# Optimization experiments

Hardware: AMD Instinct MI355X
Metric: run time of the kernel (lower is better)

## Reference

```python
import jax, jax.numpy as jnp
import numpy as np

PENALTY_FACTOR = 2.0
THRESHOLD = 0.01
PHASE_INT_THRESHOLD = 0.01  # hard-coded 0.01 in the original forward


def setup_inputs() -> dict:
    key = jax.random.key(0)
    k1, k2, k3 = jax.random.split(key, 3)
    B, twoN = 1024, 65536
    prediction = jax.random.normal(k1, (B, twoN), dtype=jnp.float32)
    label = jax.random.normal(k2, (B, twoN), dtype=jnp.float32)
    spectrogram = jax.random.normal(k3, (B, 128, 128), dtype=jnp.float32)
    return {"prediction": prediction, "label": label, "spectrogram": spectrogram}


def _significant_bounds(mask, n):
    # mask: [B, N] bool. first/last index where mask is True; (0, n-1) if none.
    idx = jnp.arange(n)
    any_ = jnp.any(mask, axis=1, keepdims=True)
    first = jnp.min(jnp.where(mask, idx, n), axis=1, keepdims=True)
    last = jnp.max(jnp.where(mask, idx, -1), axis=1, keepdims=True)
    first = jnp.where(any_, first, 0)
    last = jnp.where(any_, last, n - 1)
    return first, last  # each [B, 1]


def reference(prediction, label, spectrogram):
    B, two_n = label.shape
    n = two_n // 2
    label_real, label_imag = label[:, :n], label[:, n:]
    pred_real, pred_imag = prediction[:, :n], prediction[:, n:]

    label_phase = jnp.arctan2(label_imag, label_real)
    pred_phase = jnp.arctan2(pred_imag, pred_real)
    label_int = label_real ** 2 + label_imag ** 2
    pred_int = pred_real ** 2 + pred_imag ** 2

    idx = jnp.arange(n)[None, :]  # [1, N]
    fr, lr = _significant_bounds(jnp.abs(label_real) > THRESHOLD, n)
    fi, li = _significant_bounds(jnp.abs(label_imag) > THRESHOLD, n)

    # penalty applied outside the significant region [first, last]
    scale_r = jnp.where((idx < fr) | (idx > lr), PENALTY_FACTOR, 1.0)
    scale_i = jnp.where((idx < fi) | (idx > li), PENALTY_FACTOR, 1.0)

    mse_real = (pred_real - label_real) ** 2 * scale_r
    mse_imag = (pred_imag - label_imag) ** 2 * scale_i
    mse_int = (pred_int - label_int) ** 2
    mse_phase = jnp.where(jnp.abs(label_int) < PHASE_INT_THRESHOLD,
                          0.0, (pred_phase - label_phase) ** 2)

    per_sample = (mse_real.mean(axis=1) + mse_imag.mean(axis=1)
                  + 10.0 * mse_int.mean(axis=1) + 5.0 * mse_phase.mean(axis=1))
    return per_sample.mean()
```

## Files before the change

kernel.cpp:

```cpp
#include <hip/hip_runtime.h>
#include <math.h>

#define SIG_THRESHOLD 0.01f
#define PHASE_INT_THR 0.01f

__device__ __forceinline__ float fast_atan2f(float y, float x) {
    float ax = fabsf(x), ay = fabsf(y);
    float mx = fmaxf(ax, ay), mn = fminf(ax, ay);
    float t = mn * __builtin_amdgcn_rcpf(mx);
    t = (mx == 0.0f) ? 0.0f : t;
    float s = t * t;
    float p =        -0.01172120f;
    p = fmaf(s, p,    0.05265332f);
    p = fmaf(s, p,   -0.11643287f);
    p = fmaf(s, p,    0.19354346f);
    p = fmaf(s, p,   -0.33262347f);
    p = fmaf(s, p,    0.99997726f);
    float r = p * t;
    r = (ay > ax) ? (1.57079632679f - r) : r;
    r = (x < 0.0f) ? (3.14159265359f - r) : r;
    return copysignf(r, y);
}


__device__ __forceinline__ float waveReduceSum(float v) {
#pragma unroll
    for (int o = 32; o > 0; o >>= 1) v += __shfl_down(v, o, 64);
    return v;
}
__device__ __forceinline__ int waveReduceMin(int v) {
#pragma unroll
    for (int o = 32; o > 0; o >>= 1) v = min(v, __shfl_down(v, o, 64));
    return v;
}
__device__ __forceinline__ int waveReduceMax(int v) {
#pragma unroll
    for (int o = 32; o > 0; o >>= 1) v = max(v, __shfl_down(v, o, 64));
    return v;
}

__device__ __forceinline__ float blockReduceSum(float v, float* lds) {
    __syncthreads();
    v = waveReduceSum(v);
    int lane = threadIdx.x & 63, wave = threadIdx.x >> 6;
    if (lane == 0) lds[wave] = v;
    __syncthreads();
    int nw = (blockDim.x + 63) >> 6;
    float r = (threadIdx.x < nw) ? lds[threadIdx.x] : 0.0f;
    if (threadIdx.x < 64) r = waveReduceSum(r);
    if (threadIdx.x == 0) lds[0] = r;
    __syncthreads();
    return lds[0];
}
__device__ __forceinline__ int blockReduceMin(int v, int* lds) {
    __syncthreads();
    v = waveReduceMin(v);
    int lane = threadIdx.x & 63, wave = threadIdx.x >> 6;
    if (lane == 0) lds[wave] = v;
    __syncthreads();
    int nw = (blockDim.x + 63) >> 6;
    int r = (threadIdx.x < nw) ? lds[threadIdx.x] : 0x7fffffff;
    if (threadIdx.x < 64) r = waveReduceMin(r);
    if (threadIdx.x == 0) lds[0] = r;
    __syncthreads();
    return lds[0];
}
__device__ __forceinline__ int blockReduceMax(int v, int* lds) {
    __syncthreads();
    v = waveReduceMax(v);
    int lane = threadIdx.x & 63, wave = threadIdx.x >> 6;
    if (lane == 0) lds[wave] = v;
    __syncthreads();
    int nw = (blockDim.x + 63) >> 6;
    int r = (threadIdx.x < nw) ? lds[threadIdx.x] : (int)0x80000000;
    if (threadIdx.x < 64) r = waveReduceMax(r);
    if (threadIdx.x == 0) lds[0] = r;
    __syncthreads();
    return lds[0];
}

#define COARSE_SENT (1 << 29)

__device__ __forceinline__ void process4(float4 lrv, float4 liv, float4 prv, float4 piv,
                                         int v,
                                         float& sum_r, float& sum_i, float& sum_int, float& sum_ph,
                                         int& cfr4, int& clr4, int& cfi4, int& cli4) {
#pragma unroll
    for (int k = 0; k < 4; ++k) {
        float lrk = (&lrv.x)[k], lik = (&liv.x)[k];
        float prk = (&prv.x)[k], pik = (&piv.x)[k];

        float dr = prk - lrk;  sum_r += dr * dr;
        float di = pik - lik;  sum_i += di * di;

        float lint = fmaf(lrk, lrk, lik * lik);
        float pint = fmaf(prk, prk, pik * pik);
        float dint = pint - lint;  sum_int += dint * dint;

        float dph = fast_atan2f(pik, prk) - fast_atan2f(lik, lrk);
        sum_ph += (lint >= PHASE_INT_THR) ? dph * dph : 0.0f;
    }
    float amr = fmaxf(fmaxf(fabsf(lrv.x), fabsf(lrv.y)), fmaxf(fabsf(lrv.z), fabsf(lrv.w)));
    float ami = fmaxf(fmaxf(fabsf(liv.x), fabsf(liv.y)), fmaxf(fabsf(liv.z), fabsf(liv.w)));
    bool sr = amr > SIG_THRESHOLD;
    bool si = ami > SIG_THRESHOLD;
    cfr4 = min(cfr4, sr ? v : COARSE_SENT);
    clr4 = sr ? v : clr4;
    cfi4 = min(cfi4, si ? v : COARSE_SENT);
    cli4 = si ? v : cli4;
}

__global__ void __launch_bounds__(512)
prl_row_kernel(const float* __restrict__ pred, const float* __restrict__ label,
               float* __restrict__ row_out, int n, int two_n) {
    __shared__ float s_f[16];
    __shared__ int s_i[16];
    __shared__ int s_b[4];

    const int row = blockIdx.x;
    const float* __restrict__ P = pred  + (size_t)row * two_n;
    const float* __restrict__ L = label + (size_t)row * two_n;

    const int tid = threadIdx.x;
    const int nt  = blockDim.x;

    const float4* __restrict__ Lr4 = reinterpret_cast<const float4*>(L);
    const float4* __restrict__ Li4 = reinterpret_cast<const float4*>(L + n);
    const float4* __restrict__ Pr4 = reinterpret_cast<const float4*>(P);
    const float4* __restrict__ Pi4 = reinterpret_cast<const float4*>(P + n);

    float sum_r = 0.f, sum_i = 0.f, sum_int = 0.f, sum_ph = 0.f;
    int cfr4 = COARSE_SENT, clr4 = -1, cfi4 = COARSE_SENT, cli4 = -1;

    const int nvec  = n / 4;
    const int iters = nvec / (2 * nt);
    int v = tid;
    for (int it = 0; it < iters; ++it, v += 2 * nt) {
        const int v1 = v + nt;
        float4 a0 = Lr4[v],  b0 = Li4[v],  c0 = Pr4[v],  d0 = Pi4[v];
        float4 a1 = Lr4[v1], b1 = Li4[v1], c1 = Pr4[v1], d1 = Pi4[v1];
        process4(a0, b0, c0, d0, v,  sum_r, sum_i, sum_int, sum_ph, cfr4, clr4, cfi4, cli4);
        process4(a1, b1, c1, d1, v1, sum_r, sum_i, sum_int, sum_ph, cfr4, clr4, cfi4, cli4);
    }

    float tot_r   = blockReduceSum(sum_r, s_f);
    float tot_i   = blockReduceSum(sum_i, s_f);
    float tot_int = blockReduceSum(sum_int, s_f);
    float tot_ph  = blockReduceSum(sum_ph, s_f);

    int fr4 = blockReduceMin(cfr4, s_i);
    int lr4 = blockReduceMax(clr4, s_i);
    int fi4 = blockReduceMin(cfi4, s_i);
    int li4 = blockReduceMax(cli4, s_i);

    if (tid < 4) s_b[tid] = (tid & 1) ? -1 : n;
    __syncthreads();
    if (tid < 16) {
        int which = tid >> 2;
        int k = tid & 3;
        const float* base = (which >= 2) ? (L + n) : L;
        int v4 = (which == 0) ? fr4 : (which == 1) ? lr4 : (which == 2) ? fi4 : li4;
        bool valid = (which & 1) ? (v4 >= 0) : (v4 < COARSE_SENT);
        if (valid) {
            int idx = v4 * 4 + k;
            if (fabsf(base[idx]) > SIG_THRESHOLD) {
                if (which & 1) atomicMax(&s_b[which], idx);
                else           atomicMin(&s_b[which], idx);
            }
        }
    }
    __syncthreads();
    int fr = s_b[0], lr = s_b[1], fi = s_b[2], li = s_b[3];
    if (fr == n) { fr = 0; lr = n - 1; }
    if (fi == n) { fi = 0; li = n - 1; }

    float o_r = 0.f, o_i = 0.f;
    for (int i = tid; i < fr; i += nt)          { float d = P[i] - L[i];         o_r += d * d; }
    for (int i = lr + 1 + tid; i < n; i += nt)  { float d = P[i] - L[i];         o_r += d * d; }
    for (int i = tid; i < fi; i += nt)          { float d = P[n + i] - L[n + i]; o_i += d * d; }
    for (int i = li + 1 + tid; i < n; i += nt)  { float d = P[n + i] - L[n + i]; o_i += d * d; }

    float tot_or = blockReduceSum(o_r, s_f);
    float tot_oi = blockReduceSum(o_i, s_f);

    if (tid == 0) {
        float wr = tot_r + tot_or;
        float wi = tot_i + tot_oi;
        float per_sample = (wr + wi + 10.0f * tot_int + 5.0f * tot_ph) / (float)n;
        row_out[row] = per_sample;
    }
}

__global__ void __launch_bounds__(1024)
prl_finalize_kernel(const float* __restrict__ rows, float* __restrict__ out, int B) {
    __shared__ float s_f[16];
    float v = 0.f;
    for (int i = threadIdx.x; i < B; i += blockDim.x) v += rows[i];
    float t = blockReduceSum(v, s_f);
    if (threadIdx.x == 0) out[0] = t / (float)B;
}

extern "C" void kernel_launch(void* const* d_in, const int* in_sizes, int n_in,
                              void* d_out, int out_size, void* d_ws, size_t ws_size,
                              hipStream_t stream) {
    const float* pred  = (const float*)d_in[0];
    const float* label = (const float*)d_in[1];

    const int B     = in_sizes[2] / (128 * 128);
    const int two_n = in_sizes[0] / B;
    const int n     = two_n / 2;

    float* row_out = (float*)d_ws;
    float* out     = (float*)d_out;

    prl_row_kernel<<<B, 512, 0, stream>>>(pred, label, row_out, n, two_n);
    prl_finalize_kernel<<<1, 1024, 0, stream>>>(row_out, out, B);
}
```

Baseline: 114.1 us.

## Software-pipeline row loads and compute phase difference with a single atan2

```diff
diff --git a/kernel.cpp b/kernel.cpp
--- a/kernel.cpp
+++ b/kernel.cpp
@@ -3,6 +3,7 @@
 
 #define SIG_THRESHOLD 0.01f
 #define PHASE_INT_THR 0.01f
+#define TWO_PI_F 6.283185307179586f
 
 __device__ __forceinline__ float fast_atan2f(float y, float x) {
     float ax = fabsf(x), ay = fabsf(y);
@@ -90,14 +91,21 @@
         float lrk = (&lrv.x)[k], lik = (&liv.x)[k];
         float prk = (&prv.x)[k], pik = (&piv.x)[k];
 
-        float dr = prk - lrk;  sum_r += dr * dr;
-        float di = pik - lik;  sum_i += di * di;
+        float dr = prk - lrk;  sum_r = fmaf(dr, dr, sum_r);
+        float di = pik - lik;  sum_i = fmaf(di, di, sum_i);
 
         float lint = fmaf(lrk, lrk, lik * lik);
         float pint = fmaf(prk, prk, pik * pik);
-        float dint = pint - lint;  sum_int += dint * dint;
-
-        float dph = fast_atan2f(pik, prk) - fast_atan2f(lik, lrk);
+        float dint = pint - lint;  sum_int = fmaf(dint, dint, sum_int);
+
+        float cross = fmaf(pik, lrk, -(prk * lik));
+        float dotv  = fmaf(prk, lrk,   pik * lik);
+        float w = fast_atan2f(cross, dotv);
+        bool php = pik > 0.0f;
+        bool phl = lik > 0.0f;
+        float sigma = (php && !phl && w < 0.0f) ?  1.0f
+                    : ((!php && phl && w > 0.0f) ? -1.0f : 0.0f);
+        float dph = fmaf(sigma, TWO_PI_F, w);
         sum_ph += (lint >= PHASE_INT_THR) ? dph * dph : 0.0f;
     }
     float amr = fmaxf(fmaxf(fabsf(lrv.x), fabsf(lrv.y)), fmaxf(fabsf(lrv.z), fabsf(lrv.w)));
@@ -110,38 +118,14 @@
     cli4 = si ? v : cli4;
 }
 
-__global__ void __launch_bounds__(512)
-prl_row_kernel(const float* __restrict__ pred, const float* __restrict__ label,
-               float* __restrict__ row_out, int n, int two_n) {
-    __shared__ float s_f[16];
-    __shared__ int s_i[16];
-    __shared__ int s_b[4];
-
-    const int row = blockIdx.x;
-    const float* __restrict__ P = pred  + (size_t)row * two_n;
-    const float* __restrict__ L = label + (size_t)row * two_n;
-
+__device__ __forceinline__ void row_epilogue(const float* __restrict__ P,
+                                             const float* __restrict__ L,
+                                             float* __restrict__ row_out, int row, int n,
+                                             float sum_r, float sum_i, float sum_int, float sum_ph,
+                                             int cfr4, int clr4, int cfi4, int cli4,
+                                             float* s_f, int* s_i, int* s_b) {
     const int tid = threadIdx.x;
     const int nt  = blockDim.x;
-
-    const float4* __restrict__ Lr4 = reinterpret_cast<const float4*>(L);
-    const float4* __restrict__ Li4 = reinterpret_cast<const float4*>(L + n);
-    const float4* __restrict__ Pr4 = reinterpret_cast<const float4*>(P);
-    const float4* __restrict__ Pi4 = reinterpret_cast<const float4*>(P + n);
-
-    float sum_r = 0.f, sum_i = 0.f, sum_int = 0.f, sum_ph = 0.f;
-    int cfr4 = COARSE_SENT, clr4 = -1, cfi4 = COARSE_SENT, cli4 = -1;
-
-    const int nvec  = n / 4;
-    const int iters = nvec / (2 * nt);
-    int v = tid;
-    for (int it = 0; it < iters; ++it, v += 2 * nt) {
-        const int v1 = v + nt;
-        float4 a0 = Lr4[v],  b0 = Li4[v],  c0 = Pr4[v],  d0 = Pi4[v];
-        float4 a1 = Lr4[v1], b1 = Li4[v1], c1 = Pr4[v1], d1 = Pi4[v1];
-        process4(a0, b0, c0, d0, v,  sum_r, sum_i, sum_int, sum_ph, cfr4, clr4, cfi4, cli4);
-        process4(a1, b1, c1, d1, v1, sum_r, sum_i, sum_int, sum_ph, cfr4, clr4, cfi4, cli4);
-    }
 
     float tot_r   = blockReduceSum(sum_r, s_f);
     float tot_i   = blockReduceSum(sum_i, s_f);
@@ -186,9 +170,86 @@
     if (tid == 0) {
         float wr = tot_r + tot_or;
         float wi = tot_i + tot_oi;
-        float per_sample = (wr + wi + 10.0f * tot_int + 5.0f * tot_ph) / (float)n;
-        row_out[row] = per_sample;
-    }
+        row_out[row] = (wr + wi + 10.0f * tot_int + 5.0f * tot_ph) / (float)n;
+    }
+}
+
+template<int NT, int ITERS>
+__global__ void __launch_bounds__(NT, 4)
+prl_row_fast(const float* __restrict__ pred, const float* __restrict__ label,
+             float* __restrict__ row_out, int n, int two_n) {
+    __shared__ float s_f[16];
+    __shared__ int s_i[16];
+    __shared__ int s_b[4];
+
+    const int row = blockIdx.x;
+    const float* __restrict__ P = pred  + (size_t)row * two_n;
+    const float* __restrict__ L = label + (size_t)row * two_n;
+    const int tid = threadIdx.x;
+
+    const float4* __restrict__ Lr4 = reinterpret_cast<const float4*>(L);
+    const float4* __restrict__ Li4 = reinterpret_cast<const float4*>(L + n);
+    const float4* __restrict__ Pr4 = reinterpret_cast<const float4*>(P);
+    const float4* __restrict__ Pi4 = reinterpret_cast<const float4*>(P + n);
+
+    float sum_r = 0.f, sum_i = 0.f, sum_int = 0.f, sum_ph = 0.f;
+    int cfr4 = COARSE_SENT, clr4 = -1, cfi4 = COARSE_SENT, cli4 = -1;
+
+    int v = tid;
+    float4 a0 = Lr4[v],      b0 = Li4[v],      c0 = Pr4[v],      d0 = Pi4[v];
+    float4 a1 = Lr4[v + NT], b1 = Li4[v + NT], c1 = Pr4[v + NT], d1 = Pi4[v + NT];
+
+#pragma unroll
+    for (int it = 0; it < ITERS; ++it) {
+        float4 na0 = a0, nb0 = b0, nc0 = c0, nd0 = d0;
+        float4 na1 = a1, nb1 = b1, nc1 = c1, nd1 = d1;
+        if (it + 1 < ITERS) {
+            const int vn  = v + 2 * NT;
+            const int vn1 = vn + NT;
+            na0 = Lr4[vn];  nb0 = Li4[vn];  nc0 = Pr4[vn];  nd0 = Pi4[vn];
+            na1 = Lr4[vn1]; nb1 = Li4[vn1]; nc1 = Pr4[vn1]; nd1 = Pi4[vn1];
+        }
+        __builtin_amdgcn_sched_barrier(0);
+        process4(a0, b0, c0, d0, v,      sum_r, sum_i, sum_int, sum_ph, cfr4, clr4, cfi4, cli4);
+        process4(a1, b1, c1, d1, v + NT, sum_r, sum_i, sum_int, sum_ph, cfr4, clr4, cfi4, cli4);
+        a0 = na0; b0 = nb0; c0 = nc0; d0 = nd0;
+        a1 = na1; b1 = nb1; c1 = nc1; d1 = nd1;
+        v += 2 * NT;
+    }
+
+    row_epilogue(P, L, row_out, row, n, sum_r, sum_i, sum_int, sum_ph,
+                 cfr4, clr4, cfi4, cli4, s_f, s_i, s_b);
+}
+
+__global__ void __launch_bounds__(512)
+prl_row_generic(const float* __restrict__ pred, const float* __restrict__ label,
+                float* __restrict__ row_out, int n, int two_n) {
+    __shared__ float s_f[16];
+    __shared__ int s_i[16];
+    __shared__ int s_b[4];
+
+    const int row = blockIdx.x;
+    const float* __restrict__ P = pred  + (size_t)row * two_n;
+    const float* __restrict__ L = label + (size_t)row * two_n;
+    const int tid = threadIdx.x;
+    const int nt  = blockDim.x;
+
+    const float4* __restrict__ Lr4 = reinterpret_cast<const float4*>(L);
+    const float4* __restrict__ Li4 = reinterpret_cast<const float4*>(L + n);
+    const float4* __restrict__ Pr4 = reinterpret_cast<const float4*>(P);
+    const float4* __restrict__ Pi4 = reinterpret_cast<const float4*>(P + n);
+
+    float sum_r = 0.f, sum_i = 0.f, sum_int = 0.f, sum_ph = 0.f;
+    int cfr4 = COARSE_SENT, clr4 = -1, cfi4 = COARSE_SENT, cli4 = -1;
+
+    const int nvec = n / 4;
+    for (int v = tid; v < nvec; v += nt) {
+        float4 a = Lr4[v], b = Li4[v], c = Pr4[v], d = Pi4[v];
+        process4(a, b, c, d, v, sum_r, sum_i, sum_int, sum_ph, cfr4, clr4, cfi4, cli4);
+    }
+
+    row_epilogue(P, L, row_out, row, n, sum_r, sum_i, sum_int, sum_ph,
+                 cfr4, clr4, cfi4, cli4, s_f, s_i, s_b);
 }
 
 __global__ void __launch_bounds__(1024)
@@ -213,6 +274,11 @@
     float* row_out = (float*)d_ws;
     float* out     = (float*)d_out;
 
-    prl_row_kernel<<<B, 512, 0, stream>>>(pred, label, row_out, n, two_n);
+    constexpr int NT = 512, ITERS = 8;
+    if (n == NT * ITERS * 8) {
+        prl_row_fast<NT, ITERS><<<B, NT, 0, stream>>>(pred, label, row_out, n, two_n);
+    } else {
+        prl_row_generic<<<B, 512, 0, stream>>>(pred, label, row_out, n, two_n);
+    }
     prl_finalize_kernel<<<1, 1024, 0, stream>>>(row_out, out, B);
 }
```

Result: slower. 221.7 us (+94.2%).

## Compute phase difference with a single atan2 and batch block reductions

Applied to the files above, without the earlier changes.

```diff
diff --git a/kernel.cpp b/kernel.cpp
--- a/kernel.cpp
+++ b/kernel.cpp
@@ -3,6 +3,7 @@
 
 #define SIG_THRESHOLD 0.01f
 #define PHASE_INT_THR 0.01f
+#define TWO_PI_F 6.283185307179586f
 
 __device__ __forceinline__ float fast_atan2f(float y, float x) {
     float ax = fabsf(x), ay = fabsf(y);
@@ -23,104 +24,105 @@
 }
 
 
-__device__ __forceinline__ float waveReduceSum(float v) {
+__device__ __forceinline__ float4 waveReduceSum4(float4 v) {
 #pragma unroll
-    for (int o = 32; o > 0; o >>= 1) v += __shfl_down(v, o, 64);
+    for (int o = 32; o > 0; o >>= 1) {
+        v.x += __shfl_down(v.x, o, 64);
+        v.y += __shfl_down(v.y, o, 64);
+        v.z += __shfl_down(v.z, o, 64);
+        v.w += __shfl_down(v.w, o, 64);
+    }
     return v;
 }
-__device__ __forceinline__ int waveReduceMin(int v) {
+
+__device__ __forceinline__ int4 waveReduceBounds(int4 v) {
 #pragma unroll
-    for (int o = 32; o > 0; o >>= 1) v = min(v, __shfl_down(v, o, 64));
+    for (int o = 32; o > 0; o >>= 1) {
+        v.x = min(v.x, __shfl_down(v.x, o, 64));
+        v.y = max(v.y, __shfl_down(v.y, o, 64));
+        v.z = min(v.z, __shfl_down(v.z, o, 64));
+        v.w = max(v.w, __shfl_down(v.w, o, 64));
+    }
     return v;
 }
-__device__ __forceinline__ int waveReduceMax(int v) {
-#pragma unroll
-    for (int o = 32; o > 0; o >>= 1) v = max(v, __shfl_down(v, o, 64));
-    return v;
-}
-
-__device__ __forceinline__ float blockReduceSum(float v, float* lds) {
-    __syncthreads();
-    v = waveReduceSum(v);
+
+__device__ __forceinline__ float4 blockReduceSum4(float4 v, float4* lds4) {
+    __syncthreads();
+    v = waveReduceSum4(v);
     int lane = threadIdx.x & 63, wave = threadIdx.x >> 6;
-    if (lane == 0) lds[wave] = v;
-    __syncthreads();
-    int nw = (blockDim.x + 63) >> 6;
-    float r = (threadIdx.x < nw) ? lds[threadIdx.x] : 0.0f;
-    if (threadIdx.x < 64) r = waveReduceSum(r);
-    if (threadIdx.x == 0) lds[0] = r;
-    __syncthreads();
-    return lds[0];
-}
-__device__ __forceinline__ int blockReduceMin(int v, int* lds) {
-    __syncthreads();
-    v = waveReduceMin(v);
+    if (lane == 0) lds4[wave] = v;
+    __syncthreads();
+    int nw = blockDim.x >> 6;
+    float4 r = (threadIdx.x < nw) ? lds4[threadIdx.x] : make_float4(0.f, 0.f, 0.f, 0.f);
+    if (threadIdx.x < 64) r = waveReduceSum4(r);
+    if (threadIdx.x == 0) lds4[0] = r;
+    __syncthreads();
+    return lds4[0];
+}
+
+#define COARSE_SENT (1 << 29)
+
+__device__ __forceinline__ int4 blockReduceBounds(int4 v, int4* ldsi4) {
+    __syncthreads();
+    v = waveReduceBounds(v);
     int lane = threadIdx.x & 63, wave = threadIdx.x >> 6;
-    if (lane == 0) lds[wave] = v;
-    __syncthreads();
-    int nw = (blockDim.x + 63) >> 6;
-    int r = (threadIdx.x < nw) ? lds[threadIdx.x] : 0x7fffffff;
-    if (threadIdx.x < 64) r = waveReduceMin(r);
-    if (threadIdx.x == 0) lds[0] = r;
-    __syncthreads();
-    return lds[0];
-}
-__device__ __forceinline__ int blockReduceMax(int v, int* lds) {
-    __syncthreads();
-    v = waveReduceMax(v);
-    int lane = threadIdx.x & 63, wave = threadIdx.x >> 6;
-    if (lane == 0) lds[wave] = v;
-    __syncthreads();
-    int nw = (blockDim.x + 63) >> 6;
-    int r = (threadIdx.x < nw) ? lds[threadIdx.x] : (int)0x80000000;
-    if (threadIdx.x < 64) r = waveReduceMax(r);
-    if (threadIdx.x == 0) lds[0] = r;
-    __syncthreads();
-    return lds[0];
-}
-
-#define COARSE_SENT (1 << 29)
+    if (lane == 0) ldsi4[wave] = v;
+    __syncthreads();
+    int nw = blockDim.x >> 6;
+    int4 r = (threadIdx.x < nw) ? ldsi4[threadIdx.x]
+                                : make_int4(COARSE_SENT, -1, COARSE_SENT, -1);
+    if (threadIdx.x < 64) r = waveReduceBounds(r);
+    if (threadIdx.x == 0) ldsi4[0] = r;
+    __syncthreads();
+    return ldsi4[0];
+}
 
 __device__ __forceinline__ void process4(float4 lrv, float4 liv, float4 prv, float4 piv,
                                          int v,
-                                         float& sum_r, float& sum_i, float& sum_int, float& sum_ph,
-                                         int& cfr4, int& clr4, int& cfi4, int& cli4) {
+                                         float4& sums,
+                                         int4& bounds) {
 #pragma unroll
     for (int k = 0; k < 4; ++k) {
         float lrk = (&lrv.x)[k], lik = (&liv.x)[k];
         float prk = (&prv.x)[k], pik = (&piv.x)[k];
 
-        float dr = prk - lrk;  sum_r += dr * dr;
-        float di = pik - lik;  sum_i += di * di;
+        float dr = prk - lrk;  sums.x = fmaf(dr, dr, sums.x);
+        float di = pik - lik;  sums.y = fmaf(di, di, sums.y);
 
         float lint = fmaf(lrk, lrk, lik * lik);
         float pint = fmaf(prk, prk, pik * pik);
-        float dint = pint - lint;  sum_int += dint * dint;
-
-        float dph = fast_atan2f(pik, prk) - fast_atan2f(lik, lrk);
-        sum_ph += (lint >= PHASE_INT_THR) ? dph * dph : 0.0f;
+        float dint = pint - lint;  sums.z = fmaf(dint, dint, sums.z);
+
+        float cross = fmaf(pik, lrk, -(prk * lik));
+        float dotv  = fmaf(prk, lrk,   pik * lik);
+        float w = fast_atan2f(cross, dotv);
+        bool php = pik > 0.0f;
+        bool phl = lik > 0.0f;
+        float sigma = (php && !phl && w < 0.0f) ?  1.0f
+                    : ((!php && phl && w > 0.0f) ? -1.0f : 0.0f);
+        float dph = fmaf(sigma, TWO_PI_F, w);
+        sums.w += (lint >= PHASE_INT_THR) ? dph * dph : 0.0f;
     }
     float amr = fmaxf(fmaxf(fabsf(lrv.x), fabsf(lrv.y)), fmaxf(fabsf(lrv.z), fabsf(lrv.w)));
     float ami = fmaxf(fmaxf(fabsf(liv.x), fabsf(liv.y)), fmaxf(fabsf(liv.z), fabsf(liv.w)));
     bool sr = amr > SIG_THRESHOLD;
     bool si = ami > SIG_THRESHOLD;
-    cfr4 = min(cfr4, sr ? v : COARSE_SENT);
-    clr4 = sr ? v : clr4;
-    cfi4 = min(cfi4, si ? v : COARSE_SENT);
-    cli4 = si ? v : cli4;
+    bounds.x = min(bounds.x, sr ? v : COARSE_SENT);
+    bounds.y = sr ? v : bounds.y;
+    bounds.z = min(bounds.z, si ? v : COARSE_SENT);
+    bounds.w = si ? v : bounds.w;
 }
 
 __global__ void __launch_bounds__(512)
 prl_row_kernel(const float* __restrict__ pred, const float* __restrict__ label,
                float* __restrict__ row_out, int n, int two_n) {
-    __shared__ float s_f[16];
-    __shared__ int s_i[16];
+    __shared__ float4 s_f4[8];
+    __shared__ int4 s_i4[8];
     __shared__ int s_b[4];
 
     const int row = blockIdx.x;
     const float* __restrict__ P = pred  + (size_t)row * two_n;
     const float* __restrict__ L = label + (size_t)row * two_n;
-
     const int tid = threadIdx.x;
     const int nt  = blockDim.x;
 
@@ -129,29 +131,17 @@
     const float4* __restrict__ Pr4 = reinterpret_cast<const float4*>(P);
     const float4* __restrict__ Pi4 = reinterpret_cast<const float4*>(P + n);
 
-    float sum_r = 0.f, sum_i = 0.f, sum_int = 0.f, sum_ph = 0.f;
-    int cfr4 = COARSE_SENT, clr4 = -1, cfi4 = COARSE_SENT, cli4 = -1;
-
-    const int nvec  = n / 4;
-    const int iters = nvec / (2 * nt);
-    int v = tid;
-    for (int it = 0; it < iters; ++it, v += 2 * nt) {
-        const int v1 = v + nt;
-        float4 a0 = Lr4[v],  b0 = Li4[v],  c0 = Pr4[v],  d0 = Pi4[v];
-        float4 a1 = Lr4[v1], b1 = Li4[v1], c1 = Pr4[v1], d1 = Pi4[v1];
-        process4(a0, b0, c0, d0, v,  sum_r, sum_i, sum_int, sum_ph, cfr4, clr4, cfi4, cli4);
-        process4(a1, b1, c1, d1, v1, sum_r, sum_i, sum_int, sum_ph, cfr4, clr4, cfi4, cli4);
-    }
-
-    float tot_r   = blockReduceSum(sum_r, s_f);
-    float tot_i   = blockReduceSum(sum_i, s_f);
-    float tot_int = blockReduceSum(sum_int, s_f);
-    float tot_ph  = blockReduceSum(sum_ph, s_f);
-
-    int fr4 = blockReduceMin(cfr4, s_i);
-    int lr4 = blockReduceMax(clr4, s_i);
-    int fi4 = blockReduceMin(cfi4, s_i);
-    int li4 = blockReduceMax(cli4, s_i);
+    float4 sums = make_float4(0.f, 0.f, 0.f, 0.f);
+    int4 bounds = make_int4(COARSE_SENT, -1, COARSE_SENT, -1);
+
+    const int nvec = n / 4;
+    for (int v = tid; v < nvec; v += nt) {
+        float4 a = Lr4[v], b = Li4[v], c = Pr4[v], d = Pi4[v];
+        process4(a, b, c, d, v, sums, bounds);
+    }
+
+    float4 tot = blockReduceSum4(sums, s_f4);
+    int4 b4 = blockReduceBounds(bounds, s_i4);
 
     if (tid < 4) s_b[tid] = (tid & 1) ? -1 : n;
     __syncthreads();
@@ -159,7 +149,7 @@
         int which = tid >> 2;
         int k = tid & 3;
         const float* base = (which >= 2) ? (L + n) : L;
-        int v4 = (which == 0) ? fr4 : (which == 1) ? lr4 : (which == 2) ? fi4 : li4;
+        int v4 = (which == 0) ? b4.x : (which == 1) ? b4.y : (which == 2) ? b4.z : b4.w;
         bool valid = (which & 1) ? (v4 >= 0) : (v4 < COARSE_SENT);
         if (valid) {
             int idx = v4 * 4 + k;
@@ -174,30 +164,35 @@
     if (fr == n) { fr = 0; lr = n - 1; }
     if (fi == n) { fi = 0; li = n - 1; }
 
-    float o_r = 0.f, o_i = 0.f;
-    for (int i = tid; i < fr; i += nt)          { float d = P[i] - L[i];         o_r += d * d; }
-    for (int i = lr + 1 + tid; i < n; i += nt)  { float d = P[i] - L[i];         o_r += d * d; }
-    for (int i = tid; i < fi; i += nt)          { float d = P[n + i] - L[n + i]; o_i += d * d; }
-    for (int i = li + 1 + tid; i < n; i += nt)  { float d = P[n + i] - L[n + i]; o_i += d * d; }
-
-    float tot_or = blockReduceSum(o_r, s_f);
-    float tot_oi = blockReduceSum(o_i, s_f);
+    float4 osum = make_float4(0.f, 0.f, 0.f, 0.f);
+    for (int i = tid; i < fr; i += nt)          { float d = P[i] - L[i];         osum.x = fmaf(d, d, osum.x); }
+    for (int i = lr + 1 + tid; i < n; i += nt)  { float d = P[i] - L[i];         osum.x = fmaf(d, d, osum.x); }
+    for (int i = tid; i < fi; i += nt)          { float d = P[n + i] - L[n + i]; osum.y = fmaf(d, d, osum.y); }
+    for (int i = li + 1 + tid; i < n; i += nt)  { float d = P[n + i] - L[n + i]; osum.y = fmaf(d, d, osum.y); }
+
+    float4 otot = blockReduceSum4(osum, s_f4);
 
     if (tid == 0) {
-        float wr = tot_r + tot_or;
-        float wi = tot_i + tot_oi;
-        float per_sample = (wr + wi + 10.0f * tot_int + 5.0f * tot_ph) / (float)n;
-        row_out[row] = per_sample;
+        float wr = tot.x + otot.x;
+        float wi = tot.y + otot.y;
+        row_out[row] = (wr + wi + 10.0f * tot.z + 5.0f * tot.w) / (float)n;
     }
 }
 
 __global__ void __launch_bounds__(1024)
 prl_finalize_kernel(const float* __restrict__ rows, float* __restrict__ out, int B) {
-    __shared__ float s_f[16];
-    float v = 0.f;
-    for (int i = threadIdx.x; i < B; i += blockDim.x) v += rows[i];
-    float t = blockReduceSum(v, s_f);
-    if (threadIdx.x == 0) out[0] = t / (float)B;
+    __shared__ float4 s_f4[16];
+    float4 v = make_float4(0.f, 0.f, 0.f, 0.f);
+    for (int i = threadIdx.x; i < B; i += blockDim.x) v.x += rows[i];
+    __syncthreads();
+    v = waveReduceSum4(v);
+    int lane = threadIdx.x & 63, wave = threadIdx.x >> 6;
+    if (lane == 0) s_f4[wave] = v;
+    __syncthreads();
+    int nw = blockDim.x >> 6;
+    float4 r = (threadIdx.x < nw) ? s_f4[threadIdx.x] : make_float4(0.f, 0.f, 0.f, 0.f);
+    if (threadIdx.x < 64) r = waveReduceSum4(r);
+    if (threadIdx.x == 0) out[0] = r.x / (float)B;
 }
 
 extern "C" void kernel_launch(void* const* d_in, const int* in_sizes, int n_in,
```

Result: faster. 108.1 us (median of 2 runs) (-5.3%).
